# Optimization experiments

Measured on AMD Instinct MI355X. Metric: run time of the kernel, lower is better.

Reference implementation:

```python
import jax, jax.numpy as jnp
import numpy as np

N_NODES = 100000


def _gcn_conv(x, W, b, src, dst, num_nodes):
    """PyG-style GCNConv: out = D^{-1/2}(A+I)D^{-1/2} (x W) + b.
    src/dst already include self-loops. Degree over dst with unit edge weights."""
    h = x @ W  # [N, F_out]
    ones = jnp.ones(dst.shape, dtype=h.dtype)
    deg = jax.ops.segment_sum(ones, dst, num_segments=num_nodes)  # [N]
    dinv = jnp.where(deg > 0, jax.lax.rsqrt(deg), 0.0)
    norm = dinv[src] * dinv[dst]  # [E]
    msgs = norm[:, None] * h[src]  # [E, F_out] gather
    agg = jax.ops.segment_sum(msgs, dst, num_segments=num_nodes)  # scatter-add
    return agg + b


def setup_inputs() -> dict:
    key = jax.random.key(0)
    ks = jax.random.split(key, 8)
    N, E = N_NODES, 1600000
    F_in, H, F_out = 128, 128, 64
    x = jax.random.normal(ks[0], (N, F_in), dtype=jnp.float32)
    edge_index = jax.random.randint(ks[1], (2, E), 0, N, dtype=jnp.int32)
    s_in = 1.0 / np.sqrt(F_in)
    s_h = 1.0 / np.sqrt(H)
    s_o = 1.0 / np.sqrt(F_out)
    W1 = jax.random.uniform(ks[2], (F_in, H), jnp.float32, -s_in, s_in)
    b1 = jnp.zeros((H,), jnp.float32)
    W2 = jax.random.uniform(ks[3], (H, F_out), jnp.float32, -s_h, s_h)
    b2 = jnp.zeros((F_out,), jnp.float32)
    Wout = jax.random.uniform(ks[4], (F_out, 1), jnp.float32, -s_o, s_o)
    bout = jax.random.uniform(ks[5], (1,), jnp.float32, -s_o, s_o)
    return {"x": x, "edge_index": edge_index, "W1": W1, "b1": b1,
            "W2": W2, "b2": b2, "Wout": Wout, "bout": bout}


def reference(x, edge_index, W1, b1, W2, b2, Wout, bout):
    N = x.shape[0]
    loops = jnp.arange(N, dtype=edge_index.dtype)
    src = jnp.concatenate([edge_index[0], loops])  # add self-loops
    dst = jnp.concatenate([edge_index[1], loops])
    h = jax.nn.relu(_gcn_conv(x, W1, b1, src, dst, N))
    h = jax.nn.relu(_gcn_conv(h, W2, b2, src, dst, N))
    return h @ Wout + bout  # [N, 1]
```

## Files before the change

### kernel.cpp

```cpp
#include <hip/hip_runtime.h>
#include <math.h>

#define NN 100000
#define CAP 64

typedef _Float16 hv2 __attribute__((ext_vector_type(2)));
typedef _Float16 hv4 __attribute__((ext_vector_type(4)));


__global__ __launch_bounds__(256) void k_fillg(const int* __restrict__ src,
                                               const int* __restrict__ dst,
                                               int* __restrict__ cursor,
                                               int* __restrict__ csr, int E,
                                               const float* __restrict__ x,
                                               const float* __restrict__ W,
                                               _Float16* __restrict__ hs, int M) {
    __shared__ float xt[64][132];
    int bid = blockIdx.x;
    int tid = threadIdx.x;
    if (bid % 5 != 0) {
        int fid = bid - bid / 5 - 1;
        if (fid >= 6250) return;
        int e = fid * 256 + tid;
        if (e < E) {
            int d = dst[e];
            int p = atomicAdd(&cursor[d], 1);
            if (p < CAP) csr[(size_t)d * CAP + p] = src[e];
        }
        return;
    }
    int gid = bid / 5;
    int row0 = gid * 64;
    #pragma unroll
    for (int it = 0; it < 8; ++it) {
        int idx = it * 256 + tid;
        int r = idx >> 5;
        int c4 = (idx & 31) << 2;
        float4 v = make_float4(0.f, 0.f, 0.f, 0.f);
        if (row0 + r < M) v = *(const float4*)&x[(size_t)(row0 + r) * 128 + c4];
        *(float4*)&xt[r][c4] = v;
    }
    __syncthreads();
    int ct = tid & 31, rt = tid >> 5;
    int c0 = ct * 4, r0 = rt * 8;
    float acc[8][4];
    #pragma unroll
    for (int i = 0; i < 8; ++i)
        #pragma unroll
        for (int j = 0; j < 4; ++j) acc[i][j] = 0.f;

    for (int k = 0; k < 128; k += 4) {
        float4 w0 = *(const float4*)&W[(size_t)(k + 0) * 128 + c0];
        float4 w1 = *(const float4*)&W[(size_t)(k + 1) * 128 + c0];
        float4 w2 = *(const float4*)&W[(size_t)(k + 2) * 128 + c0];
        float4 w3 = *(const float4*)&W[(size_t)(k + 3) * 128 + c0];
        #pragma unroll
        for (int i = 0; i < 8; ++i) {
            float4 xv = *(const float4*)&xt[r0 + i][k];
            acc[i][0] += xv.x * w0.x + xv.y * w1.x + xv.z * w2.x + xv.w * w3.x;
            acc[i][1] += xv.x * w0.y + xv.y * w1.y + xv.z * w2.y + xv.w * w3.y;
            acc[i][2] += xv.x * w0.z + xv.y * w1.z + xv.z * w2.z + xv.w * w3.z;
            acc[i][3] += xv.x * w0.w + xv.y * w1.w + xv.z * w2.w + xv.w * w3.w;
        }
    }
    #pragma unroll
    for (int i = 0; i < 8; ++i) {
        int r = row0 + r0 + i;
        if (r < M) {
            hv4 o;
            o.x = (_Float16)acc[i][0];
            o.y = (_Float16)acc[i][1];
            o.z = (_Float16)acc[i][2];
            o.w = (_Float16)acc[i][3];
            *(hv4*)&hs[(size_t)r * 128 + c0] = o;
        }
    }
}


__global__ __launch_bounds__(256) void k_dinvscale(const int* __restrict__ cursor,
                                                   float* __restrict__ dinv,
                                                   _Float16* __restrict__ hs, int n) {
    __shared__ float ds[64];
    int tid = threadIdx.x;
    int row0 = blockIdx.x * 64;
    if (tid < 64) {
        int r = row0 + tid;
        float dv = 0.f;
        if (r < n) {
            dv = rsqrtf((float)(cursor[r] + 1));
            dinv[r] = dv;
        }
        ds[tid] = dv;
    }
    __syncthreads();
    int w = tid >> 6, lane = tid & 63;
    for (int i = w; i < 64; i += 4) {
        int r = row0 + i;
        if (r >= n) break;
        float dv = ds[i];
        hv2* p = (hv2*)&hs[(size_t)r * 128 + 2 * lane];
        hv2 v = *p;
        v.x = (_Float16)((float)v.x * dv);
        v.y = (_Float16)((float)v.y * dv);
        *p = v;
    }
}


__global__ __launch_bounds__(256) void k_agg1(const _Float16* __restrict__ hs,
                                              const int* __restrict__ csr,
                                              const int* __restrict__ deg,
                                              const float* __restrict__ dinv,
                                              const float* __restrict__ b,
                                              _Float16* __restrict__ out, int n) {
    int wave = (blockIdx.x * 256 + threadIdx.x) >> 6;
    int lane = threadIdx.x & 63;
    if (wave >= n) return;
    int node = wave;
    int start = node * CAP;
    int cnt   = __builtin_amdgcn_readfirstlane(deg[node]);
    cnt = cnt < CAP ? cnt : CAP;
    const _Float16* gbase = hs + 2 * lane;

    hv2 sv = *(const hv2*)(gbase + (size_t)node * 128);
    float2 av[4];
    av[0] = make_float2((float)sv.x, (float)sv.y);
    av[1] = make_float2(0.f, 0.f);
    av[2] = make_float2(0.f, 0.f);
    av[3] = make_float2(0.f, 0.f);

    int j = 0;
    for (; j + 16 <= cnt; j += 16) {
        int s[16];
        #pragma unroll
        for (int u = 0; u < 16; ++u) s[u] = csr[start + j + u];
        hv2 v[16];
        #pragma unroll
        for (int u = 0; u < 16; ++u) v[u] = *(const hv2*)(gbase + (size_t)s[u] * 128);
        #pragma unroll
        for (int u = 0; u < 16; ++u) {
            av[u & 3].x += (float)v[u].x;
            av[u & 3].y += (float)v[u].y;
        }
    }
    for (; j + 4 <= cnt; j += 4) {
        int s[4];
        #pragma unroll
        for (int u = 0; u < 4; ++u) s[u] = csr[start + j + u];
        hv2 v[4];
        #pragma unroll
        for (int u = 0; u < 4; ++u) v[u] = *(const hv2*)(gbase + (size_t)s[u] * 128);
        #pragma unroll
        for (int u = 0; u < 4; ++u) {
            av[u].x += (float)v[u].x;
            av[u].y += (float)v[u].y;
        }
    }
    for (; j < cnt; ++j) {
        int s0 = csr[start + j];
        hv2 v0 = *(const hv2*)(gbase + (size_t)s0 * 128);
        av[0].x += (float)v0.x;
        av[0].y += (float)v0.y;
    }
    float ax = (av[0].x + av[1].x) + (av[2].x + av[3].x);
    float ay = (av[0].y + av[1].y) + (av[2].y + av[3].y);

    float d = dinv[node];
    hv2 o;
    o.x = (_Float16)fmaxf(d * ax + b[2 * lane], 0.f);
    o.y = (_Float16)fmaxf(d * ay + b[2 * lane + 1], 0.f);
    __builtin_nontemporal_store(o, (hv2*)&out[(size_t)node * 128 + 2 * lane]);
}


__global__ __launch_bounds__(256) void k_gemm2(const _Float16* __restrict__ a,
                                               const float* __restrict__ W,
                                               const float* __restrict__ dinv,
                                               _Float16* __restrict__ hs, int M) {
    __shared__ float xt[64][132];
    int tid = threadIdx.x;
    int row0 = blockIdx.x * 64;
    #pragma unroll
    for (int it = 0; it < 8; ++it) {
        int idx = it * 256 + tid;
        int r = idx >> 5;
        int c4 = (idx & 31) << 2;
        float4 v = make_float4(0.f, 0.f, 0.f, 0.f);
        if (row0 + r < M) {
            hv4 hvv = *(const hv4*)&a[(size_t)(row0 + r) * 128 + c4];
            v = make_float4((float)hvv.x, (float)hvv.y, (float)hvv.z, (float)hvv.w);
        }
        *(float4*)&xt[r][c4] = v;
    }
    __syncthreads();
    int ct = tid & 15, rt = tid >> 4;
    int c0 = ct * 4, r0 = rt * 4;
    float acc[4][4];
    #pragma unroll
    for (int i = 0; i < 4; ++i)
        #pragma unroll
        for (int j = 0; j < 4; ++j) acc[i][j] = 0.f;

    for (int k = 0; k < 128; k += 4) {
        float4 w0 = *(const float4*)&W[(size_t)(k + 0) * 64 + c0];
        float4 w1 = *(const float4*)&W[(size_t)(k + 1) * 64 + c0];
        float4 w2 = *(const float4*)&W[(size_t)(k + 2) * 64 + c0];
        float4 w3 = *(const float4*)&W[(size_t)(k + 3) * 64 + c0];
        #pragma unroll
        for (int i = 0; i < 4; ++i) {
            float4 xv = *(const float4*)&xt[r0 + i][k];
            acc[i][0] += xv.x * w0.x + xv.y * w1.x + xv.z * w2.x + xv.w * w3.x;
            acc[i][1] += xv.x * w0.y + xv.y * w1.y + xv.z * w2.y + xv.w * w3.y;
            acc[i][2] += xv.x * w0.z + xv.y * w1.z + xv.z * w2.z + xv.w * w3.z;
            acc[i][3] += xv.x * w0.w + xv.y * w1.w + xv.z * w2.w + xv.w * w3.w;
        }
    }
    #pragma unroll
    for (int i = 0; i < 4; ++i) {
        int r = row0 + r0 + i;
        if (r < M) {
            float d = dinv[r];
            hv4 o;
            o.x = (_Float16)(acc[i][0] * d);
            o.y = (_Float16)(acc[i][1] * d);
            o.z = (_Float16)(acc[i][2] * d);
            o.w = (_Float16)(acc[i][3] * d);
            *(hv4*)&hs[(size_t)r * 64 + c0] = o;
        }
    }
}


__global__ __launch_bounds__(256) void k_agg2(const _Float16* __restrict__ hs,
                                              const int* __restrict__ csr,
                                              const int* __restrict__ deg,
                                              const float* __restrict__ dinv,
                                              const float* __restrict__ b2,
                                              const float* __restrict__ Wout,
                                              const float* __restrict__ bout,
                                              float* __restrict__ out, int n) {
    int wave = (blockIdx.x * 256 + threadIdx.x) >> 6;
    int lane = threadIdx.x & 63;
    if (wave >= n) return;
    int node = wave;
    int start = node * CAP;
    int cnt   = __builtin_amdgcn_readfirstlane(deg[node]);
    cnt = cnt < CAP ? cnt : CAP;
    const _Float16* base = hs + lane;

    float av[4];
    av[0] = (float)base[(size_t)node * 64];
    av[1] = 0.f; av[2] = 0.f; av[3] = 0.f;

    int j = 0;
    for (; j + 16 <= cnt; j += 16) {
        int s[16];
        #pragma unroll
        for (int u = 0; u < 16; ++u) s[u] = csr[start + j + u];
        float v[16];
        #pragma unroll
        for (int u = 0; u < 16; ++u) v[u] = (float)base[(size_t)s[u] * 64];
        #pragma unroll
        for (int u = 0; u < 16; ++u) av[u & 3] += v[u];
    }
    for (; j + 4 <= cnt; j += 4) {
        int s[4];
        #pragma unroll
        for (int u = 0; u < 4; ++u) s[u] = csr[start + j + u];
        float v[4];
        #pragma unroll
        for (int u = 0; u < 4; ++u) v[u] = (float)base[(size_t)s[u] * 64];
        #pragma unroll
        for (int u = 0; u < 4; ++u) av[u] += v[u];
    }
    for (; j < cnt; ++j) {
        av[0] += (float)base[(size_t)csr[start + j] * 64];
    }
    float acc = (av[0] + av[1]) + (av[2] + av[3]);

    float d = dinv[node];
    float a2 = fmaxf(d * acc + b2[lane], 0.f);
    float p = a2 * Wout[lane];
    #pragma unroll
    for (int off = 32; off > 0; off >>= 1) p += __shfl_down(p, off, 64);
    if (lane == 0) __builtin_nontemporal_store(p + bout[0], &out[node]);
}


extern "C" void kernel_launch(void* const* d_in, const int* in_sizes, int n_in,
                              void* d_out, int out_size, void* d_ws, size_t ws_size,
                              hipStream_t stream) {
    const float* x    = (const float*)d_in[0];
    const int*   ei   = (const int*)d_in[1];
    const float* W1   = (const float*)d_in[2];
    const float* b1   = (const float*)d_in[3];
    const float* W2   = (const float*)d_in[4];
    const float* b2   = (const float*)d_in[5];
    const float* Wout = (const float*)d_in[6];
    const float* bout = (const float*)d_in[7];

    const int N = NN;
    const int E = in_sizes[1] / 2;
    const int* src = ei;
    const int* dst = ei + E;

    char* ws = (char*)d_ws;
    size_t off = 0;
    auto alloc = [&](size_t bytes) -> void* {
        void* p = ws + off;
        off = (off + bytes + 255) & ~(size_t)255;
        return p;
    };
    int*      cursor = (int*)alloc((size_t)N * 4);
    float*    dinv   = (float*)alloc((size_t)N * 4);
    int*      csr    = (int*)alloc((size_t)N * CAP * 4);
    _Float16* hs1    = (_Float16*)alloc((size_t)N * 128 * 2);
    _Float16* a1     = (_Float16*)alloc((size_t)N * 128 * 2);
    _Float16* hs2    = (_Float16*)alloc((size_t)N * 64 * 2);

    (void)hipMemsetAsync(cursor, 0, (size_t)N * 4, stream);

    k_fillg<<<7815, 256, 0, stream>>>(src, dst, cursor, csr, E, x, W1, hs1, N);
    k_dinvscale<<<(N + 63) / 64, 256, 0, stream>>>(cursor, dinv, hs1, N);
    k_agg1 <<<(N + 3) / 4, 256, 0, stream>>>(hs1, csr, cursor, dinv, b1, a1, N);
    k_gemm2<<<(N + 63) / 64, 256, 0, stream>>>(a1, W2, dinv, hs2, N);
    k_agg2 <<<(N + 3) / 4, 256, 0, stream>>>(hs2, csr, cursor, dinv, b2, Wout, bout,
                                             (float*)d_out, N);
}
```

Measured before the change: 267.9 us.

## Shard CSR fill counters per XCC and fold dinv scaling into aggregation

Edge bucketing now uses eight sub-counters per node, one per XCC read from a hardware register, with overflow spilling to the next sub-bucket. This cuts cross-die atomic contention on a shared cursor. The separate dinv-scaling kernel is replaced by a small degree-summing kernel, and layer-1 aggregation now multiplies each neighbor by its own dinv while gathering. The aggregation loops walk the 8 sub-buckets without the previous 16-wide unrolled batching, which may reduce memory-level parallelism and adds a per-neighbor dinv load. The work split in the fill kernel changes from 1:4 gemm:fill blocks to 1:1, with each fill block handling 1024 edges.

```diff
diff --git a/kernel.cpp b/kernel.cpp
--- a/kernel.cpp
+++ b/kernel.cpp
@@ -2,15 +2,20 @@
 #include <math.h>
 
 #define NN 100000
-#define CAP 64
+#define NSUB 8
+#define CAPX 16
 
 typedef _Float16 hv2 __attribute__((ext_vector_type(2)));
 typedef _Float16 hv4 __attribute__((ext_vector_type(4)));
 
+__device__ __forceinline__ int xcc_id() {
+    return (int)(__builtin_amdgcn_s_getreg(20 | (0 << 6) | (3 << 11)) & 7u);
+}
+
 
 __global__ __launch_bounds__(256) void k_fillg(const int* __restrict__ src,
                                                const int* __restrict__ dst,
-                                               int* __restrict__ cursor,
+                                               int* __restrict__ cur,
                                                int* __restrict__ csr, int E,
                                                const float* __restrict__ x,
                                                const float* __restrict__ W,
@@ -18,18 +23,29 @@
     __shared__ float xt[64][132];
     int bid = blockIdx.x;
     int tid = threadIdx.x;
-    if (bid % 5 != 0) {
-        int fid = bid - bid / 5 - 1;
-        if (fid >= 6250) return;
-        int e = fid * 256 + tid;
-        if (e < E) {
-            int d = dst[e];
-            int p = atomicAdd(&cursor[d], 1);
-            if (p < CAP) csr[(size_t)d * CAP + p] = src[e];
+    if (bid & 1) {
+        int fid = bid >> 1;
+        int sub0 = xcc_id();
+        int e0 = fid * 1024 + tid;
+        #pragma unroll
+        for (int k = 0; k < 4; ++k) {
+            int e = e0 + k * 256;
+            if (e < E) {
+                int d = dst[e];
+                int s = src[e];
+                int sub = sub0;
+                int p = atomicAdd(&cur[sub * NN + d], 1);
+                #pragma unroll 1
+                for (int t = 0; t < 7 && p >= CAPX; ++t) {
+                    sub = (sub + 1) & 7;
+                    p = atomicAdd(&cur[sub * NN + d], 1);
+                }
+                if (p < CAPX) csr[(size_t)d * 128 + sub * CAPX + p] = s;
+            }
         }
         return;
     }
-    int gid = bid / 5;
+    int gid = bid >> 1;
     int row0 = gid * 64;
     #pragma unroll
     for (int it = 0; it < 8; ++it) {
@@ -78,39 +94,25 @@
 }
 
 
-__global__ __launch_bounds__(256) void k_dinvscale(const int* __restrict__ cursor,
-                                                   float* __restrict__ dinv,
-                                                   _Float16* __restrict__ hs, int n) {
-    __shared__ float ds[64];
-    int tid = threadIdx.x;
-    int row0 = blockIdx.x * 64;
-    if (tid < 64) {
-        int r = row0 + tid;
-        float dv = 0.f;
-        if (r < n) {
-            dv = rsqrtf((float)(cursor[r] + 1));
-            dinv[r] = dv;
-        }
-        ds[tid] = dv;
-    }
-    __syncthreads();
-    int w = tid >> 6, lane = tid & 63;
-    for (int i = w; i < 64; i += 4) {
-        int r = row0 + i;
-        if (r >= n) break;
-        float dv = ds[i];
-        hv2* p = (hv2*)&hs[(size_t)r * 128 + 2 * lane];
-        hv2 v = *p;
-        v.x = (_Float16)((float)v.x * dv);
-        v.y = (_Float16)((float)v.y * dv);
-        *p = v;
+__global__ void k_deg(const int* __restrict__ cur, int* __restrict__ deg,
+                      float* __restrict__ dinv, int n) {
+    int i = blockIdx.x * 256 + threadIdx.x;
+    if (i < n) {
+        int s = 0;
+        #pragma unroll
+        for (int k = 0; k < NSUB; ++k) {
+            int c = cur[k * NN + i];
+            s += (c < CAPX ? c : CAPX);
+        }
+        deg[i] = s;
+        dinv[i] = rsqrtf((float)(s + 1));
     }
 }
 
 
 __global__ __launch_bounds__(256) void k_agg1(const _Float16* __restrict__ hs,
                                               const int* __restrict__ csr,
-                                              const int* __restrict__ deg,
+                                              const int* __restrict__ cur,
                                               const float* __restrict__ dinv,
                                               const float* __restrict__ b,
                                               _Float16* __restrict__ out, int n) {
@@ -118,58 +120,37 @@
     int lane = threadIdx.x & 63;
     if (wave >= n) return;
     int node = wave;
-    int start = node * CAP;
-    int cnt   = __builtin_amdgcn_readfirstlane(deg[node]);
-    cnt = cnt < CAP ? cnt : CAP;
+    int c[NSUB];
+    int maxc = 0;
+    #pragma unroll
+    for (int k = 0; k < NSUB; ++k) {
+        int v = __builtin_amdgcn_readfirstlane(cur[k * NN + node]);
+        v = v < CAPX ? v : CAPX;
+        c[k] = v;
+        maxc = maxc > v ? maxc : v;
+    }
     const _Float16* gbase = hs + 2 * lane;
+    const int* crow = csr + (size_t)node * 128;
+    float dn = dinv[node];
 
     hv2 sv = *(const hv2*)(gbase + (size_t)node * 128);
-    float2 av[4];
-    av[0] = make_float2((float)sv.x, (float)sv.y);
-    av[1] = make_float2(0.f, 0.f);
-    av[2] = make_float2(0.f, 0.f);
-    av[3] = make_float2(0.f, 0.f);
-
-    int j = 0;
-    for (; j + 16 <= cnt; j += 16) {
-        int s[16];
-        #pragma unroll
-        for (int u = 0; u < 16; ++u) s[u] = csr[start + j + u];
-        hv2 v[16];
-        #pragma unroll
-        for (int u = 0; u < 16; ++u) v[u] = *(const hv2*)(gbase + (size_t)s[u] * 128);
-        #pragma unroll
-        for (int u = 0; u < 16; ++u) {
-            av[u & 3].x += (float)v[u].x;
-            av[u & 3].y += (float)v[u].y;
-        }
-    }
-    for (; j + 4 <= cnt; j += 4) {
-        int s[4];
-        #pragma unroll
-        for (int u = 0; u < 4; ++u) s[u] = csr[start + j + u];
-        hv2 v[4];
-        #pragma unroll
-        for (int u = 0; u < 4; ++u) v[u] = *(const hv2*)(gbase + (size_t)s[u] * 128);
-        #pragma unroll
-        for (int u = 0; u < 4; ++u) {
-            av[u].x += (float)v[u].x;
-            av[u].y += (float)v[u].y;
-        }
-    }
-    for (; j < cnt; ++j) {
-        int s0 = csr[start + j];
-        hv2 v0 = *(const hv2*)(gbase + (size_t)s0 * 128);
-        av[0].x += (float)v0.x;
-        av[0].y += (float)v0.y;
-    }
-    float ax = (av[0].x + av[1].x) + (av[2].x + av[3].x);
-    float ay = (av[0].y + av[1].y) + (av[2].y + av[3].y);
-
-    float d = dinv[node];
+    float ax = dn * (float)sv.x, ay = dn * (float)sv.y;
+
+    for (int p = 0; p < maxc; ++p) {
+        #pragma unroll
+        for (int k = 0; k < NSUB; ++k) {
+            if (p < c[k]) {
+                int s = __builtin_amdgcn_readfirstlane(crow[k * CAPX + p]);
+                float ds = dinv[s];
+                hv2 v = *(const hv2*)(gbase + (size_t)s * 128);
+                ax += ds * (float)v.x;
+                ay += ds * (float)v.y;
+            }
+        }
+    }
     hv2 o;
-    o.x = (_Float16)fmaxf(d * ax + b[2 * lane], 0.f);
-    o.y = (_Float16)fmaxf(d * ay + b[2 * lane + 1], 0.f);
+    o.x = (_Float16)fmaxf(dn * ax + b[2 * lane], 0.f);
+    o.y = (_Float16)fmaxf(dn * ay + b[2 * lane + 1], 0.f);
     __builtin_nontemporal_store(o, (hv2*)&out[(size_t)node * 128 + 2 * lane]);
 }
 
@@ -234,7 +215,7 @@
 
 __global__ __launch_bounds__(256) void k_agg2(const _Float16* __restrict__ hs,
                                               const int* __restrict__ csr,
-                                              const int* __restrict__ deg,
+                                              const int* __restrict__ cur,
                                               const float* __restrict__ dinv,
                                               const float* __restrict__ b2,
                                               const float* __restrict__ Wout,
@@ -244,47 +225,34 @@
     int lane = threadIdx.x & 63;
     if (wave >= n) return;
     int node = wave;
-    int start = node * CAP;
-    int cnt   = __builtin_amdgcn_readfirstlane(deg[node]);
-    cnt = cnt < CAP ? cnt : CAP;
+    int c[NSUB];
+    int maxc = 0;
+    #pragma unroll
+    for (int k = 0; k < NSUB; ++k) {
+        int v = __builtin_amdgcn_readfirstlane(cur[k * NN + node]);
+        v = v < CAPX ? v : CAPX;
+        c[k] = v;
+        maxc = maxc > v ? maxc : v;
+    }
     const _Float16* base = hs + lane;
-
-    float av[4];
-    av[0] = (float)base[(size_t)node * 64];
-    av[1] = 0.f; av[2] = 0.f; av[3] = 0.f;
-
-    int j = 0;
-    for (; j + 16 <= cnt; j += 16) {
-        int s[16];
-        #pragma unroll
-        for (int u = 0; u < 16; ++u) s[u] = csr[start + j + u];
-        float v[16];
-        #pragma unroll
-        for (int u = 0; u < 16; ++u) v[u] = (float)base[(size_t)s[u] * 64];
-        #pragma unroll
-        for (int u = 0; u < 16; ++u) av[u & 3] += v[u];
-    }
-    for (; j + 4 <= cnt; j += 4) {
-        int s[4];
-        #pragma unroll
-        for (int u = 0; u < 4; ++u) s[u] = csr[start + j + u];
-        float v[4];
-        #pragma unroll
-        for (int u = 0; u < 4; ++u) v[u] = (float)base[(size_t)s[u] * 64];
-        #pragma unroll
-        for (int u = 0; u < 4; ++u) av[u] += v[u];
-    }
-    for (; j < cnt; ++j) {
-        av[0] += (float)base[(size_t)csr[start + j] * 64];
-    }
-    float acc = (av[0] + av[1]) + (av[2] + av[3]);
-
-    float d = dinv[node];
-    float a2 = fmaxf(d * acc + b2[lane], 0.f);
-    float p = a2 * Wout[lane];
-    #pragma unroll
-    for (int off = 32; off > 0; off >>= 1) p += __shfl_down(p, off, 64);
-    if (lane == 0) __builtin_nontemporal_store(p + bout[0], &out[node]);
+    const int* crow = csr + (size_t)node * 128;
+
+    float a0 = (float)base[(size_t)node * 64];
+    for (int p = 0; p < maxc; ++p) {
+        #pragma unroll
+        for (int k = 0; k < NSUB; ++k) {
+            if (p < c[k]) {
+                int s = __builtin_amdgcn_readfirstlane(crow[k * CAPX + p]);
+                a0 += (float)base[(size_t)s * 64];
+            }
+        }
+    }
+    float dn = dinv[node];
+    float a2 = fmaxf(dn * a0 + b2[lane], 0.f);
+    float pp = a2 * Wout[lane];
+    #pragma unroll
+    for (int off = 32; off > 0; off >>= 1) pp += __shfl_down(pp, off, 64);
+    if (lane == 0) __builtin_nontemporal_store(pp + bout[0], &out[node]);
 }
 
 
@@ -312,19 +280,20 @@
         off = (off + bytes + 255) & ~(size_t)255;
         return p;
     };
-    int*      cursor = (int*)alloc((size_t)N * 4);
-    float*    dinv   = (float*)alloc((size_t)N * 4);
-    int*      csr    = (int*)alloc((size_t)N * CAP * 4);
-    _Float16* hs1    = (_Float16*)alloc((size_t)N * 128 * 2);
-    _Float16* a1     = (_Float16*)alloc((size_t)N * 128 * 2);
-    _Float16* hs2    = (_Float16*)alloc((size_t)N * 64 * 2);
-
-    (void)hipMemsetAsync(cursor, 0, (size_t)N * 4, stream);
-
-    k_fillg<<<7815, 256, 0, stream>>>(src, dst, cursor, csr, E, x, W1, hs1, N);
-    k_dinvscale<<<(N + 63) / 64, 256, 0, stream>>>(cursor, dinv, hs1, N);
-    k_agg1 <<<(N + 3) / 4, 256, 0, stream>>>(hs1, csr, cursor, dinv, b1, a1, N);
+    int*      cur  = (int*)alloc((size_t)NSUB * N * 4);
+    int*      deg  = (int*)alloc((size_t)N * 4);
+    float*    dinv = (float*)alloc((size_t)N * 4);
+    int*      csr  = (int*)alloc((size_t)N * 128 * 4);
+    _Float16* hs1  = (_Float16*)alloc((size_t)N * 128 * 2);
+    _Float16* a1   = (_Float16*)alloc((size_t)N * 128 * 2);
+    _Float16* hs2  = hs1;
+
+    (void)hipMemsetAsync(cur, 0, (size_t)NSUB * N * 4, stream);
+
+    k_fillg<<<3126, 256, 0, stream>>>(src, dst, cur, csr, E, x, W1, hs1, N);
+    k_deg  <<<(N + 255) / 256, 256, 0, stream>>>(cur, deg, dinv, N);
+    k_agg1 <<<(N + 3) / 4, 256, 0, stream>>>(hs1, csr, cur, dinv, b1, a1, N);
     k_gemm2<<<(N + 63) / 64, 256, 0, stream>>>(a1, W2, dinv, hs2, N);
-    k_agg2 <<<(N + 3) / 4, 256, 0, stream>>>(hs2, csr, cursor, dinv, b2, Wout, bout,
+    k_agg2 <<<(N + 3) / 4, 256, 0, stream>>>(hs2, csr, cur, dinv, b2, Wout, bout,
                                              (float*)d_out, N);
 }
```

Result: slower. 458.9 us (+71.3%).

## Vectorize aggregation gathers with shuffled CSR indices and rebalance fill kernel

Applied to the files above, without the earlier changes.

The aggregation kernels now load each node's CSR neighbor list once with one index per lane, then broadcast indices via shuffles. Lanes are split so several neighbors are gathered at once with 8-byte half4 loads, and the partial sums are reduced across lanes with xor shuffles. The fused fill/GEMM kernel interleaves fill and GEMM blocks 1:1 instead of 4:1, and each fill thread handles 4 edges so more atomics are in flight. The hs2 buffer aliases hs1 to reduce the workspace footprint. The aim is fewer scalar index loads and wider gather transactions, at the cost of extra shuffles and partial lane idling on the tails.

```diff
diff --git a/kernel.cpp b/kernel.cpp
--- a/kernel.cpp
+++ b/kernel.cpp
@@ -11,26 +11,37 @@
 __global__ __launch_bounds__(256) void k_fillg(const int* __restrict__ src,
                                                const int* __restrict__ dst,
                                                int* __restrict__ cursor,
-                                               int* __restrict__ csr, int E,
+                                               int* __restrict__ csr, int E, int NBF,
                                                const float* __restrict__ x,
                                                const float* __restrict__ W,
                                                _Float16* __restrict__ hs, int M) {
     __shared__ float xt[64][132];
     int bid = blockIdx.x;
     int tid = threadIdx.x;
-    if (bid % 5 != 0) {
-        int fid = bid - bid / 5 - 1;
-        if (fid >= 6250) return;
-        int e = fid * 256 + tid;
-        if (e < E) {
-            int d = dst[e];
-            int p = atomicAdd(&cursor[d], 1);
-            if (p < CAP) csr[(size_t)d * CAP + p] = src[e];
-        }
+    if (bid & 1) {
+        int fid = bid >> 1;
+        if (fid >= NBF) return;
+        int e0 = fid * 1024 + tid;
+        int dd[4], ss[4], pp[4];
+        bool ok[4];
+        #pragma unroll
+        for (int k = 0; k < 4; ++k) {
+            int e = e0 + k * 256;
+            ok[k] = (e < E);
+            dd[k] = ok[k] ? dst[e] : 0;
+            ss[k] = ok[k] ? src[e] : 0;
+        }
+        #pragma unroll
+        for (int k = 0; k < 4; ++k)
+            if (ok[k]) pp[k] = atomicAdd(&cursor[dd[k]], 1);
+        #pragma unroll
+        for (int k = 0; k < 4; ++k)
+            if (ok[k] && pp[k] < CAP) csr[(size_t)dd[k] * CAP + pp[k]] = ss[k];
         return;
     }
-    int gid = bid / 5;
+    int gid = bid >> 1;
     int row0 = gid * 64;
+    if (row0 >= M) return;
     #pragma unroll
     for (int it = 0; it < 8; ++it) {
         int idx = it * 256 + tid;
@@ -110,7 +121,7 @@
 
 __global__ __launch_bounds__(256) void k_agg1(const _Float16* __restrict__ hs,
                                               const int* __restrict__ csr,
-                                              const int* __restrict__ deg,
+                                              const int* __restrict__ cursor,
                                               const float* __restrict__ dinv,
                                               const float* __restrict__ b,
                                               _Float16* __restrict__ out, int n) {
@@ -119,58 +130,66 @@
     if (wave >= n) return;
     int node = wave;
     int start = node * CAP;
-    int cnt   = __builtin_amdgcn_readfirstlane(deg[node]);
+    int cnt = __builtin_amdgcn_readfirstlane(cursor[node]);
     cnt = cnt < CAP ? cnt : CAP;
-    const _Float16* gbase = hs + 2 * lane;
-
-    hv2 sv = *(const hv2*)(gbase + (size_t)node * 128);
-    float2 av[4];
-    av[0] = make_float2((float)sv.x, (float)sv.y);
-    av[1] = make_float2(0.f, 0.f);
-    av[2] = make_float2(0.f, 0.f);
-    av[3] = make_float2(0.f, 0.f);
+    int h = lane >> 5;
+    int f0 = 4 * (lane & 31);
+
+    int my_idx = (lane < cnt) ? csr[start + lane] : 0;
+
+    float a0[4] = {0.f, 0.f, 0.f, 0.f};
+    float a1r[4] = {0.f, 0.f, 0.f, 0.f};
 
     int j = 0;
     for (; j + 16 <= cnt; j += 16) {
-        int s[16];
-        #pragma unroll
-        for (int u = 0; u < 16; ++u) s[u] = csr[start + j + u];
-        hv2 v[16];
-        #pragma unroll
-        for (int u = 0; u < 16; ++u) v[u] = *(const hv2*)(gbase + (size_t)s[u] * 128);
-        #pragma unroll
-        for (int u = 0; u < 16; ++u) {
-            av[u & 3].x += (float)v[u].x;
-            av[u & 3].y += (float)v[u].y;
-        }
-    }
-    for (; j + 4 <= cnt; j += 4) {
-        int s[4];
-        #pragma unroll
-        for (int u = 0; u < 4; ++u) s[u] = csr[start + j + u];
-        hv2 v[4];
-        #pragma unroll
-        for (int u = 0; u < 4; ++u) v[u] = *(const hv2*)(gbase + (size_t)s[u] * 128);
-        #pragma unroll
-        for (int u = 0; u < 4; ++u) {
-            av[u].x += (float)v[u].x;
-            av[u].y += (float)v[u].y;
-        }
-    }
-    for (; j < cnt; ++j) {
-        int s0 = csr[start + j];
-        hv2 v0 = *(const hv2*)(gbase + (size_t)s0 * 128);
-        av[0].x += (float)v0.x;
-        av[0].y += (float)v0.y;
-    }
-    float ax = (av[0].x + av[1].x) + (av[2].x + av[3].x);
-    float ay = (av[0].y + av[1].y) + (av[2].y + av[3].y);
-
-    float d = dinv[node];
-    hv2 o;
-    o.x = (_Float16)fmaxf(d * ax + b[2 * lane], 0.f);
-    o.y = (_Float16)fmaxf(d * ay + b[2 * lane + 1], 0.f);
-    __builtin_nontemporal_store(o, (hv2*)&out[(size_t)node * 128 + 2 * lane]);
+        hv4 v[8];
+        #pragma unroll
+        for (int u = 0; u < 8; ++u) {
+            int s = __shfl(my_idx, j + 2 * u + h, 64);
+            v[u] = *(const hv4*)(hs + (size_t)s * 128 + f0);
+        }
+        #pragma unroll
+        for (int u = 0; u < 8; ++u) {
+            float* a = (u & 1) ? a1r : a0;
+            a[0] += (float)v[u].x; a[1] += (float)v[u].y;
+            a[2] += (float)v[u].z; a[3] += (float)v[u].w;
+        }
+    }
+    for (; j + 2 <= cnt; j += 2) {
+        int s = __shfl(my_idx, j + h, 64);
+        hv4 v = *(const hv4*)(hs + (size_t)s * 128 + f0);
+        a0[0] += (float)v.x; a0[1] += (float)v.y;
+        a0[2] += (float)v.z; a0[3] += (float)v.w;
+    }
+    if (j < cnt) {
+        int s = __shfl(my_idx, j, 64);
+        if (h == 0) {
+            hv4 v = *(const hv4*)(hs + (size_t)s * 128 + f0);
+            a0[0] += (float)v.x; a0[1] += (float)v.y;
+            a0[2] += (float)v.z; a0[3] += (float)v.w;
+        }
+    }
+    if (h == 0) {
+        hv4 v = *(const hv4*)(hs + (size_t)node * 128 + f0);
+        a0[0] += (float)v.x; a0[1] += (float)v.y;
+        a0[2] += (float)v.z; a0[3] += (float)v.w;
+    }
+
+    float tot[4];
+    #pragma unroll
+    for (int i = 0; i < 4; ++i) {
+        tot[i] = a0[i] + a1r[i];
+        tot[i] += __shfl_xor(tot[i], 32, 64);
+    }
+    float dn = dinv[node];
+    float4 bb = *(const float4*)&b[f0];
+    hv4 o;
+    o.x = (_Float16)fmaxf(dn * tot[0] + bb.x, 0.f);
+    o.y = (_Float16)fmaxf(dn * tot[1] + bb.y, 0.f);
+    o.z = (_Float16)fmaxf(dn * tot[2] + bb.z, 0.f);
+    o.w = (_Float16)fmaxf(dn * tot[3] + bb.w, 0.f);
+    if (h == 0)
+        __builtin_nontemporal_store(o, (hv4*)&out[(size_t)node * 128 + f0]);
 }
 
 
@@ -234,7 +253,7 @@
 
 __global__ __launch_bounds__(256) void k_agg2(const _Float16* __restrict__ hs,
                                               const int* __restrict__ csr,
-                                              const int* __restrict__ deg,
+                                              const int* __restrict__ cursor,
                                               const float* __restrict__ dinv,
                                               const float* __restrict__ b2,
                                               const float* __restrict__ Wout,
@@ -245,45 +264,70 @@
     if (wave >= n) return;
     int node = wave;
     int start = node * CAP;
-    int cnt   = __builtin_amdgcn_readfirstlane(deg[node]);
+    int cnt = __builtin_amdgcn_readfirstlane(cursor[node]);
     cnt = cnt < CAP ? cnt : CAP;
-    const _Float16* base = hs + lane;
-
-    float av[4];
-    av[0] = (float)base[(size_t)node * 64];
-    av[1] = 0.f; av[2] = 0.f; av[3] = 0.f;
+    int q = lane >> 4;
+    int f0 = 4 * (lane & 15);
+
+    int my_idx = (lane < cnt) ? csr[start + lane] : 0;
+
+    float a0[4] = {0.f, 0.f, 0.f, 0.f};
+    float a1r[4] = {0.f, 0.f, 0.f, 0.f};
 
     int j = 0;
     for (; j + 16 <= cnt; j += 16) {
-        int s[16];
-        #pragma unroll
-        for (int u = 0; u < 16; ++u) s[u] = csr[start + j + u];
-        float v[16];
-        #pragma unroll
-        for (int u = 0; u < 16; ++u) v[u] = (float)base[(size_t)s[u] * 64];
-        #pragma unroll
-        for (int u = 0; u < 16; ++u) av[u & 3] += v[u];
+        hv4 v[4];
+        #pragma unroll
+        for (int u = 0; u < 4; ++u) {
+            int s = __shfl(my_idx, j + 4 * u + q, 64);
+            v[u] = *(const hv4*)(hs + (size_t)s * 64 + f0);
+        }
+        #pragma unroll
+        for (int u = 0; u < 4; ++u) {
+            float* a = (u & 1) ? a1r : a0;
+            a[0] += (float)v[u].x; a[1] += (float)v[u].y;
+            a[2] += (float)v[u].z; a[3] += (float)v[u].w;
+        }
     }
     for (; j + 4 <= cnt; j += 4) {
-        int s[4];
-        #pragma unroll
-        for (int u = 0; u < 4; ++u) s[u] = csr[start + j + u];
-        float v[4];
-        #pragma unroll
-        for (int u = 0; u < 4; ++u) v[u] = (float)base[(size_t)s[u] * 64];
-        #pragma unroll
-        for (int u = 0; u < 4; ++u) av[u] += v[u];
-    }
-    for (; j < cnt; ++j) {
-        av[0] += (float)base[(size_t)csr[start + j] * 64];
-    }
-    float acc = (av[0] + av[1]) + (av[2] + av[3]);
-
-    float d = dinv[node];
-    float a2 = fmaxf(d * acc + b2[lane], 0.f);
-    float p = a2 * Wout[lane];
-    #pragma unroll
-    for (int off = 32; off > 0; off >>= 1) p += __shfl_down(p, off, 64);
+        int s = __shfl(my_idx, j + q, 64);
+        hv4 v = *(const hv4*)(hs + (size_t)s * 64 + f0);
+        a0[0] += (float)v.x; a0[1] += (float)v.y;
+        a0[2] += (float)v.z; a0[3] += (float)v.w;
+    }
+    int rem = cnt - j;
+    if (rem > 0) {
+        int s = __shfl(my_idx, j + (q < rem ? q : 0), 64);
+        if (q < rem) {
+            hv4 v = *(const hv4*)(hs + (size_t)s * 64 + f0);
+            a0[0] += (float)v.x; a0[1] += (float)v.y;
+            a0[2] += (float)v.z; a0[3] += (float)v.w;
+        }
+    }
+    if (q == 0) {
+        hv4 v = *(const hv4*)(hs + (size_t)node * 64 + f0);
+        a0[0] += (float)v.x; a0[1] += (float)v.y;
+        a0[2] += (float)v.z; a0[3] += (float)v.w;
+    }
+
+    float tot[4];
+    #pragma unroll
+    for (int i = 0; i < 4; ++i) {
+        tot[i] = a0[i] + a1r[i];
+        tot[i] += __shfl_xor(tot[i], 16, 64);
+        tot[i] += __shfl_xor(tot[i], 32, 64);
+    }
+    float dn = dinv[node];
+    float4 bb = *(const float4*)&b2[f0];
+    float4 wv = *(const float4*)&Wout[f0];
+    float p = fmaxf(dn * tot[0] + bb.x, 0.f) * wv.x
+            + fmaxf(dn * tot[1] + bb.y, 0.f) * wv.y
+            + fmaxf(dn * tot[2] + bb.z, 0.f) * wv.z
+            + fmaxf(dn * tot[3] + bb.w, 0.f) * wv.w;
+    p += __shfl_xor(p, 1, 64);
+    p += __shfl_xor(p, 2, 64);
+    p += __shfl_xor(p, 4, 64);
+    p += __shfl_xor(p, 8, 64);
     if (lane == 0) __builtin_nontemporal_store(p + bout[0], &out[node]);
 }
 
@@ -317,11 +361,14 @@
     int*      csr    = (int*)alloc((size_t)N * CAP * 4);
     _Float16* hs1    = (_Float16*)alloc((size_t)N * 128 * 2);
     _Float16* a1     = (_Float16*)alloc((size_t)N * 128 * 2);
-    _Float16* hs2    = (_Float16*)alloc((size_t)N * 64 * 2);
+    _Float16* hs2    = hs1;
 
     (void)hipMemsetAsync(cursor, 0, (size_t)N * 4, stream);
 
-    k_fillg<<<7815, 256, 0, stream>>>(src, dst, cursor, csr, E, x, W1, hs1, N);
+    int NBF = (E + 1023) / 1024;
+    int NBG = (N + 63) / 64;
+    int NB = NBF > NBG ? NBF : NBG;
+    k_fillg<<<2 * NB, 256, 0, stream>>>(src, dst, cursor, csr, E, NBF, x, W1, hs1, N);
     k_dinvscale<<<(N + 63) / 64, 256, 0, stream>>>(cursor, dinv, hs1, N);
     k_agg1 <<<(N + 3) / 4, 256, 0, stream>>>(hs1, csr, cursor, dinv, b1, a1, N);
     k_gemm2<<<(N + 63) / 64, 256, 0, stream>>>(a1, W2, dinv, hs2, N);
```

Result: faster. 253.3 us (median of 3 runs) (-5.5%).
